# Kernel tuning notes

Hardware: AMD Instinct MI355X
Metric: run time of the kernel (lower is better)

Reference implementation:

```python
import jax, jax.numpy as jnp
import numpy as np

B, T, D, H = 256, 512, 512, 512


def setup_inputs() -> dict:
    key = jax.random.key(0)
    k1, k2, k3, k4 = jax.random.split(key, 4)
    inputs = jax.random.normal(k1, (B, T, D), dtype=jnp.float32)
    lengths = jax.random.randint(k2, (B,), 0, T).astype(jnp.int32)
    # LSTM params. Flax nn.LSTMCell uses per-gate dense layers:
    #  input dense (with bias) and recurrent dense (no bias). Packing the
    #  four gates (i, f, g, o) into one matrix is mathematically identical.
    Wx = jax.random.normal(k3, (D, 4 * H), dtype=jnp.float32) * (1.0 / np.sqrt(D))
    Wh = jax.random.normal(k4, (H, 4 * H), dtype=jnp.float32) * (1.0 / np.sqrt(H))
    b = jnp.zeros((4 * H,), dtype=jnp.float32)
    return {"inputs": inputs, "lengths": lengths, "Wx": Wx, "Wh": Wh, "b": b}


def reference(inputs, lengths, Wx, Wh, b):
    batch = inputs.shape[0]
    hidden = Wh.shape[0]
    x_tbd = jnp.swapaxes(inputs, 0, 1)  # [T, B, D]

    def step(carry, x_t):
        c, h = carry
        # fused gate pre-activations: [B, 4H]
        z = x_t @ Wx + h @ Wh + b
        i, f, g, o = jnp.split(z, 4, axis=-1)
        i = jax.nn.sigmoid(i)
        f = jax.nn.sigmoid(f)
        g = jnp.tanh(g)
        o = jax.nn.sigmoid(o)
        c_new = f * c + i * g
        h_new = o * jnp.tanh(c_new)
        return (c_new, h_new), h_new

    c0 = jnp.zeros((batch, hidden), dtype=inputs.dtype)
    h0 = jnp.zeros((batch, hidden), dtype=inputs.dtype)
    _, hs = jax.lax.scan(step, (c0, h0), x_tbd)  # hs: [T, B, H]

    # select output at last valid timestep per example
    idx = jnp.maximum(0, lengths - 1)  # [B]
    return hs[idx, jnp.arange(batch), :]  # [B, H]
```

## Files before the change

### kernel.cpp

```cpp
#include <hip/hip_runtime.h>

#define Bb 256
#define Tt 512
#define Dd 512
#define Hh 512
#define KTOT 1024
#define FOURH 2048

typedef __attribute__((ext_vector_type(8))) short bf16x8;
typedef __attribute__((ext_vector_type(4))) float f32x4;

__device__ __forceinline__ unsigned short f2bf(float f) {
    union { float f; unsigned u; } x; x.f = f;
    unsigned u = x.u;
    unsigned r = u + 0x7FFFu + ((u >> 16) & 1u);
    return (unsigned short)(r >> 16);
}
__device__ __forceinline__ float bf2f(unsigned short s) {
    union { unsigned u; float f; } x; x.u = ((unsigned)s) << 16;
    return x.f;
}

__device__ __forceinline__ uint4 load16_sc01(const void* p) {
    uint4 v;
    asm volatile("global_load_dwordx4 %0, %1, off sc0 sc1" : "=v"(v) : "v"(p));
    return v;
}

__device__ __forceinline__ void i16_to_bf(int v, unsigned short& bh, unsigned short& bl) {
    int vh = v >> 8;
    int vl = v & 255;
    union { float f; unsigned u; } a, b;
    a.f = (float)vh * 0.0078125f;
    b.f = (float)vl * 3.0517578125e-05f;
    bh = (unsigned short)(a.u >> 16);
    bl = (unsigned short)(b.u >> 16);
}

__global__ void prep_w(const float* __restrict__ Wx, const float* __restrict__ Wh,
                       unsigned short* __restrict__ WT_hi, unsigned short* __restrict__ WT_lo) {
    __shared__ float tile[32][33];
    int n0 = (blockIdx.x & 63) * 32;
    int k0 = (blockIdx.x >> 6) * 32;
    int tx = threadIdx.x & 31;
    int ty = threadIdx.x >> 5;
    for (int q = 0; q < 4; ++q) {
        int k = k0 + ty + q * 8;
        int n = n0 + tx;
        float v = (k < Dd) ? Wx[(size_t)k * FOURH + n] : Wh[(size_t)(k - Dd) * FOURH + n];
        tile[ty + q * 8][tx] = v;
    }
    __syncthreads();
    for (int q = 0; q < 4; ++q) {
        int nl = ty + q * 8;
        int kl = tx;
        float v = tile[kl][nl];
        unsigned short hi = f2bf(v);
        unsigned short lo = f2bf(v - bf2f(hi));
        size_t o = (size_t)(n0 + nl) * KTOT + (size_t)(k0 + kl);
        WT_hi[o] = hi;
        WT_lo[o] = lo;
    }
}

__global__ void init_state3(char* __restrict__ ws, int persist) {
    long i = (long)blockIdx.x * blockDim.x + threadIdx.x;
    if (i < 98304) {
        *(uint4*)(ws + (8u << 20) + i * 16) = (uint4){0, 0, 0, 0};
    }
    if (persist && i < 4096) {
        ((unsigned int*)(ws + (8u << 20) + (1536u << 10)))[i] = 0u;
    }
}

__global__ __launch_bounds__(512) void lstm_persist12(
    const float* __restrict__ X, const int* __restrict__ lengths,
    const unsigned short* __restrict__ WT_hi, const unsigned short* __restrict__ WT_lo,
    const float* __restrict__ bias,
    short* __restrict__ h_i16,
    unsigned int* __restrict__ ctrl,
    float* __restrict__ out)
{
    __shared__ unsigned short HLDS[32768];
    __shared__ unsigned short XLDS[32768];
    __shared__ float zbuf[8][32][17];

    const int bx = blockIdx.x;
    const int group = bx & 7;
    const int slot = bx >> 3;
    const int rt = slot & 7;
    const int cs = slot >> 3;
    const int r0 = rt * 32;
    const int j0h = group * 64 + cs * 16;
    const int tid = threadIdx.x;
    const int w8 = tid >> 6;
    const int lane = tid & 63;
    const int l15 = lane & 15;
    const int q4 = lane >> 4;
    const int klo = q4 * 8;
    const int gate = w8 & 3;
    const int khalf = w8 >> 2;

    const size_t HB = (size_t)Bb * Hh;

    const int colg = gate * 512 + j0h + l15;
    const size_t bbase = (size_t)colg * KTOT + (size_t)khalf * 512;
    const unsigned short* bhp = &WT_hi[bbase];
    const unsigned short* blp = &WT_lo[bbase];

    const int xr = tid >> 4;
    const int xk0 = (tid & 15) * 32;
    const float* xbase = &X[((size_t)(r0 + xr) * Tt) * Dd + xk0];
    const int ksx = tid & 15;
    const int xmi = xr >> 4, xlr = xr & 15;

    const int er = tid >> 4;
    const int ej = tid & 15;
    const int row_g = r0 + er;
    const int col_h = j0h + ej;
    const size_t oidx = (size_t)row_g * Hh + col_h;
    int oT = lengths[row_g] - 1; if (oT < 0) oT = 0;
    const float b0 = bias[col_h], b1 = bias[512 + col_h],
                b2 = bias[1024 + col_h], b3 = bias[1536 + col_h];
    float creg = 0.f;

    const int wgIdx = group * 4 + cs;
    unsigned int* myflag = ctrl + ((size_t)(rt * 32 + wgIdx)) * 16;
    const unsigned int* flagbase = ctrl + (size_t)rt * 32 * 16;
    const unsigned int* pollp = flagbase + (size_t)(lane & 31) * 16;

    {
        const float* xp = xbase;
        float4 xv[8];
#pragma unroll
        for (int i = 0; i < 8; ++i) xv[i] = ((const float4*)xp)[i];
#pragma unroll
        for (int c2 = 0; c2 < 4; ++c2) {
            float vv[8];
            *(float4*)&vv[0] = xv[2 * c2];
            *(float4*)&vv[4] = xv[2 * c2 + 1];
            bf16x8 hv8, lv8;
#pragma unroll
            for (int e = 0; e < 8; ++e) {
                unsigned short hs = f2bf(vv[e]);
                hv8[e] = (short)hs;
                lv8[e] = (short)f2bf(vv[e] - bf2f(hs));
            }
            const int lnw = (c2 * 16 + xlr) ^ (ksx & 7);
            *(bf16x8*)&XLDS[(((0 * 2 + xmi) * 16 + ksx) * 64 + lnw) * 8] = hv8;
            *(bf16x8*)&XLDS[(((1 * 2 + xmi) * 16 + ksx) * 64 + lnw) * 8] = lv8;
        }
    }

    for (int t = 0; t < Tt; ++t) {
        const int p_r = t & 1;
        const short* hp_r = h_i16 + (size_t)p_r * HB;
        short* hp_w = h_i16 + (size_t)(p_r ^ 1) * HB;

        uint4 hb[4];
#pragma unroll
        for (int it = 0; it < 4; ++it) {
            const int c = it * 512 + tid;
            const int row = c >> 6, k8 = c & 63;
            hb[it] = load16_sc01(hp_r + (size_t)(r0 + row) * Hh + k8 * 8);
        }

        asm volatile("s_waitcnt vmcnt(0)" ::: "memory");
        __builtin_amdgcn_sched_barrier(0);

#pragma unroll
        for (int it = 0; it < 4; ++it) {
            const int c = it * 512 + tid;
            const int row = c >> 6, k8 = c & 63;
            const int ksh = k8 >> 2, qq = k8 & 3;
            const int mi = row >> 4, lr = row & 15;
            const uint4 q = hb[it];
            const unsigned qs[4] = {q.x, q.y, q.z, q.w};
            bf16x8 ahv, alv;
#pragma unroll
            for (int e = 0; e < 4; ++e) {
                const unsigned u = qs[e];
                unsigned short bh0, bl0, bh1, bl1;
                i16_to_bf((int)(short)(u & 0xffffu), bh0, bl0);
                i16_to_bf((int)(short)(u >> 16), bh1, bl1);
                ahv[2 * e] = (short)bh0; alv[2 * e] = (short)bl0;
                ahv[2 * e + 1] = (short)bh1; alv[2 * e + 1] = (short)bl1;
            }
            const int lnw = (qq * 16 + lr) ^ (ksh & 7);
            *(bf16x8*)&HLDS[(((0 * 2 + mi) * 16 + ksh) * 64 + lnw) * 8] = ahv;
            *(bf16x8*)&HLDS[(((1 * 2 + mi) * 16 + ksh) * 64 + lnw) * 8] = alv;
        }
        __syncthreads();

        const unsigned short* ALDS = khalf ? HLDS : XLDS;
        f32x4 acc[2][3];
#pragma unroll
        for (int mi = 0; mi < 2; ++mi)
#pragma unroll
            for (int s = 0; s < 3; ++s)
                acc[mi][s] = (f32x4){0.f, 0.f, 0.f, 0.f};

#pragma unroll
        for (int ks = 0; ks < 16; ++ks) {
            const int kk = ks * 32 + klo;
            const bf16x8 bh = *(const bf16x8*)&bhp[kk];
            const bf16x8 bl = *(const bf16x8*)&blp[kk];
            const int lnr = lane ^ (ks & 7);
#pragma unroll
            for (int mi = 0; mi < 2; ++mi) {
                const bf16x8 ah = *(const bf16x8*)&ALDS[(((0 * 2 + mi) * 16 + ks) * 64 + lnr) * 8];
                const bf16x8 al = *(const bf16x8*)&ALDS[(((1 * 2 + mi) * 16 + ks) * 64 + lnr) * 8];
                acc[mi][0] = __builtin_amdgcn_mfma_f32_16x16x32_bf16(ah, bh, acc[mi][0], 0, 0, 0);
                acc[mi][1] = __builtin_amdgcn_mfma_f32_16x16x32_bf16(ah, bl, acc[mi][1], 0, 0, 0);
                acc[mi][2] = __builtin_amdgcn_mfma_f32_16x16x32_bf16(al, bh, acc[mi][2], 0, 0, 0);
            }
        }

#pragma unroll
        for (int mi = 0; mi < 2; ++mi) {
            const f32x4 z = acc[mi][0] + acc[mi][1] + acc[mi][2];
#pragma unroll
            for (int r = 0; r < 4; ++r)
                zbuf[w8][mi * 16 + q4 * 4 + r][l15] = z[r];
        }
        __syncthreads();

        float zi = zbuf[0][er][ej] + zbuf[4][er][ej] + b0;
        float zf = zbuf[1][er][ej] + zbuf[5][er][ej] + b1;
        float zg = zbuf[2][er][ej] + zbuf[6][er][ej] + b2;
        float zo = zbuf[3][er][ej] + zbuf[7][er][ej] + b3;
        float ig = 1.f / (1.f + expf(-zi));
        float fg = 1.f / (1.f + expf(-zf));
        float gg = tanhf(zg);
        float og = 1.f / (1.f + expf(-zo));
        float cn = fg * creg + ig * gg;
        creg = cn;
        float hn = og * tanhf(cn);
        int vi = __float2int_rn(hn * 32768.f);
        vi = vi > 32767 ? 32767 : (vi < -32767 ? -32767 : vi);
        __hip_atomic_store(&hp_w[oidx], (short)vi, __ATOMIC_RELAXED, __HIP_MEMORY_SCOPE_SYSTEM);
        if (t == oT) out[oidx] = hn;

        if (t < Tt - 1) {
            asm volatile("s_waitcnt vmcnt(0)" ::: "memory");
            __syncthreads();
            if (tid == 0)
                __hip_atomic_store(myflag, (unsigned)(t + 1), __ATOMIC_RELAXED,
                                   __HIP_MEMORY_SCOPE_SYSTEM);

            {
                const float* xp = xbase + (size_t)(t + 1) * Dd;
                float4 xv[8];
#pragma unroll
                for (int i = 0; i < 8; ++i) xv[i] = ((const float4*)xp)[i];
#pragma unroll
                for (int c2 = 0; c2 < 4; ++c2) {
                    float vv[8];
                    *(float4*)&vv[0] = xv[2 * c2];
                    *(float4*)&vv[4] = xv[2 * c2 + 1];
                    bf16x8 hv8, lv8;
#pragma unroll
                    for (int e = 0; e < 8; ++e) {
                        unsigned short hs = f2bf(vv[e]);
                        hv8[e] = (short)hs;
                        lv8[e] = (short)f2bf(vv[e] - bf2f(hs));
                    }
                    const int lnw = (c2 * 16 + xlr) ^ (ksx & 7);
                    *(bf16x8*)&XLDS[(((0 * 2 + xmi) * 16 + ksx) * 64 + lnw) * 8] = hv8;
                    *(bf16x8*)&XLDS[(((1 * 2 + xmi) * 16 + ksx) * 64 + lnw) * 8] = lv8;
                }
            }

            if (w8 == 0) {
                while (true) {
                    unsigned v = __hip_atomic_load(pollp, __ATOMIC_RELAXED,
                                                   __HIP_MEMORY_SCOPE_SYSTEM);
                    if (__all(v >= (unsigned)(t + 1))) break;
                    __builtin_amdgcn_s_sleep(2);
                }
            }
            __syncthreads();
        }
    }
}

__global__ __launch_bounds__(512) void lstm_step4(
    const float* __restrict__ X, const int* __restrict__ lengths,
    const unsigned short* __restrict__ WT_hi, const unsigned short* __restrict__ WT_lo,
    const float* __restrict__ bias,
    float* __restrict__ c_st,
    const unsigned short* __restrict__ h_r_hi, const unsigned short* __restrict__ h_r_lo,
    unsigned short* __restrict__ h_w_hi, unsigned short* __restrict__ h_w_lo,
    float* __restrict__ out, int t)
{
    __shared__ float zbuf[8][16][17];

    const int bx = blockIdx.x;
    const int xcd = bx & 7;
    const int rem = bx >> 3;
    const int m0 = (rem & 15) * 16;
    const int col_group = xcd * 4 + (rem >> 4);
    const int hc0 = col_group * 16;
    const int tid = threadIdx.x;
    const int w8 = tid >> 6;
    const int lane = tid & 63;
    const int gate = w8 & 3;
    const int khalf = w8 >> 2;

    f32x4 ahh = (f32x4){0,0,0,0}, ahl = (f32x4){0,0,0,0}, alh = (f32x4){0,0,0,0};

    const int colk = gate * 512 + hc0 + (lane & 15);
    const size_t bbase = (size_t)colk * KTOT;
    const int klo = (lane >> 4) * 8;
    const int row = m0 + (lane & 15);

    if (khalf == 0) {
        const float* xrow = &X[((size_t)row * Tt + t) * Dd];
        const unsigned short* bhp = &WT_hi[bbase];
        const unsigned short* blp = &WT_lo[bbase];
#pragma unroll
        for (int ks = 0; ks < 16; ++ks) {
            const int kk = ks * 32 + klo;
            const float4 v0 = *(const float4*)&xrow[kk];
            const float4 v1 = *(const float4*)&xrow[kk + 4];
            float vv[8] = {v0.x, v0.y, v0.z, v0.w, v1.x, v1.y, v1.z, v1.w};
            bf16x8 ah, al;
#pragma unroll
            for (int e = 0; e < 8; ++e) {
                unsigned short hi = f2bf(vv[e]);
                ah[e] = (short)hi;
                al[e] = (short)f2bf(vv[e] - bf2f(hi));
            }
            const bf16x8 bh = *(const bf16x8*)&bhp[kk];
            const bf16x8 bl = *(const bf16x8*)&blp[kk];
            ahh = __builtin_amdgcn_mfma_f32_16x16x32_bf16(ah, bh, ahh, 0, 0, 0);
            ahl = __builtin_amdgcn_mfma_f32_16x16x32_bf16(ah, bl, ahl, 0, 0, 0);
            alh = __builtin_amdgcn_mfma_f32_16x16x32_bf16(al, bh, alh, 0, 0, 0);
        }
    } else {
        const unsigned short* hrh = &h_r_hi[(size_t)row * Hh];
        const unsigned short* hrl = &h_r_lo[(size_t)row * Hh];
        const unsigned short* bhp = &WT_hi[bbase + 512];
        const unsigned short* blp = &WT_lo[bbase + 512];
#pragma unroll
        for (int ks = 0; ks < 16; ++ks) {
            const int kk = ks * 32 + klo;
            const bf16x8 ah = *(const bf16x8*)&hrh[kk];
            const bf16x8 al = *(const bf16x8*)&hrl[kk];
            const bf16x8 bh = *(const bf16x8*)&bhp[kk];
            const bf16x8 bl = *(const bf16x8*)&blp[kk];
            ahh = __builtin_amdgcn_mfma_f32_16x16x32_bf16(ah, bh, ahh, 0, 0, 0);
            ahl = __builtin_amdgcn_mfma_f32_16x16x32_bf16(ah, bl, ahl, 0, 0, 0);
            alh = __builtin_amdgcn_mfma_f32_16x16x32_bf16(al, bh, alh, 0, 0, 0);
        }
    }

    const f32x4 z = ahh + ahl + alh;
#pragma unroll
    for (int r = 0; r < 4; ++r)
        zbuf[w8][(lane >> 4) * 4 + r][lane & 15] = z[r];
    __syncthreads();

    if (tid < 256) {
        const int r = tid >> 4;
        const int j = tid & 15;
        const int row_g = m0 + r;
        const int col_g = hc0 + j;
        float zi = zbuf[0][r][j] + zbuf[4][r][j] + bias[col_g];
        float zf = zbuf[1][r][j] + zbuf[5][r][j] + bias[512 + col_g];
        float zg = zbuf[2][r][j] + zbuf[6][r][j] + bias[1024 + col_g];
        float zo = zbuf[3][r][j] + zbuf[7][r][j] + bias[1536 + col_g];
        float ig = 1.f / (1.f + expf(-zi));
        float fg = 1.f / (1.f + expf(-zf));
        float gg = tanhf(zg);
        float og = 1.f / (1.f + expf(-zo));
        const size_t idx = (size_t)row_g * Hh + col_g;
        float cn = fg * c_st[idx] + ig * gg;
        float hn = og * tanhf(cn);
        c_st[idx] = cn;
        unsigned short hh = f2bf(hn);
        h_w_hi[idx] = hh;
        h_w_lo[idx] = f2bf(hn - bf2f(hh));
        int len = lengths[row_g];
        int oidx = len - 1; if (oidx < 0) oidx = 0;
        if (t == oidx) out[idx] = hn;
    }
}

extern "C" void kernel_launch(void* const* d_in, const int* in_sizes, int n_in,
                              void* d_out, int out_size, void* d_ws, size_t ws_size,
                              hipStream_t stream) {
    const float* X = (const float*)d_in[0];
    const int* lengths = (const int*)d_in[1];
    const float* Wx = (const float*)d_in[2];
    const float* Wh = (const float*)d_in[3];
    const float* bias = (const float*)d_in[4];
    float* out = (float*)d_out;

    char* ws = (char*)d_ws;
    unsigned short* WT_hi = (unsigned short*)ws;
    unsigned short* WT_lo = (unsigned short*)(ws + (4u << 20));
    short* h_i16 = (short*)(ws + (8u << 20));
    unsigned int* ctrl = (unsigned int*)(ws + (8u << 20) + (1536u << 10));
    float* c_st = (float*)(ws + (8u << 20));
    unsigned short* h_base = (unsigned short*)(ws + (8u << 20) + (512u << 10));
    const size_t HB = (size_t)Bb * Hh;
    unsigned short* h_hi0 = h_base;
    unsigned short* h_lo0 = h_base + HB;
    unsigned short* h_hi1 = h_base + 2 * HB;
    unsigned short* h_lo1 = h_base + 3 * HB;

    const size_t NEED_PERSIST = (8u << 20) + (1536u << 10) + 32768u;
    const int can_persist = (ws_size >= NEED_PERSIST) ? 1 : 0;

    hipLaunchKernelGGL(prep_w, dim3(2048), dim3(256), 0, stream, Wx, Wh, WT_hi, WT_lo);
    hipLaunchKernelGGL(init_state3, dim3(512), dim3(256), 0, stream, ws, can_persist);

    hipError_t err = hipErrorUnknown;
    if (can_persist) {
        void* args[] = { (void*)&X, (void*)&lengths, (void*)&WT_hi, (void*)&WT_lo,
                         (void*)&bias, (void*)&h_i16, (void*)&ctrl, (void*)&out };
        err = hipLaunchCooperativeKernel((const void*)lstm_persist12,
                                         dim3(256), dim3(512), args, 0, stream);
    }
    if (err != hipSuccess) {
        for (int t = 0; t < Tt; ++t) {
            const bool even = (t & 1) == 0;
            hipLaunchKernelGGL(lstm_step4, dim3(512), dim3(512), 0, stream,
                               X, lengths, WT_hi, WT_lo, bias, c_st,
                               even ? h_hi0 : h_hi1, even ? h_lo0 : h_lo1,
                               even ? h_hi1 : h_hi0, even ? h_lo1 : h_lo0,
                               out, t);
        }
    }
}
```

Baseline: 6.112 ms.

## Halve batch rows per workgroup and launch twice as many persistent blocks

The persistent LSTM kernel now gives each workgroup 16 batch rows instead of 32 and launches 512 cooperative blocks instead of 256, shrinking the LDS buffers and MFMA accumulators to match. Each step's per-block work (h load, X conversion, one MFMA tile per wave) is halved, so more CUs share the serial recurrence. In exchange there are twice as many flags to poll and sync across blocks, half the threads sit idle during the gate math, and each block reloads the same weight slice for less work. The launch bound of 4 blocks per CU is set so the cooperative grid can be co-resident.

Result: slower. 8.250 ms (+35.0%).

```diff
diff --git a/kernel.cpp b/kernel.cpp
--- a/kernel.cpp
+++ b/kernel.cpp
@@ -68,12 +68,12 @@
     if (i < 98304) {
         *(uint4*)(ws + (8u << 20) + i * 16) = (uint4){0, 0, 0, 0};
     }
-    if (persist && i < 4096) {
+    if (persist && i < 8192) {
         ((unsigned int*)(ws + (8u << 20) + (1536u << 10)))[i] = 0u;
     }
 }
 
-__global__ __launch_bounds__(512) void lstm_persist12(
+__global__ __launch_bounds__(512, 4) void lstm_persist18(
     const float* __restrict__ X, const int* __restrict__ lengths,
     const unsigned short* __restrict__ WT_hi, const unsigned short* __restrict__ WT_lo,
     const float* __restrict__ bias,
@@ -81,16 +81,15 @@
     unsigned int* __restrict__ ctrl,
     float* __restrict__ out)
 {
-    __shared__ unsigned short HLDS[32768];
-    __shared__ unsigned short XLDS[32768];
-    __shared__ float zbuf[8][32][17];
+    __shared__ unsigned short HLDS[16384];
+    __shared__ unsigned short XLDS[16384];
+    __shared__ float zbuf[8][16][17];
 
     const int bx = blockIdx.x;
     const int group = bx & 7;
-    const int slot = bx >> 3;
-    const int rt = slot & 7;
-    const int cs = slot >> 3;
-    const int r0 = rt * 32;
+    const int cs = (bx >> 3) & 3;
+    const int rt = bx >> 5;
+    const int r0 = rt * 16;
     const int j0h = group * 64 + cs * 16;
     const int tid = threadIdx.x;
     const int w8 = tid >> 6;
@@ -108,18 +107,17 @@
     const unsigned short* bhp = &WT_hi[bbase];
     const unsigned short* blp = &WT_lo[bbase];
 
-    const int xr = tid >> 4;
-    const int xk0 = (tid & 15) * 32;
-    const float* xbase = &X[((size_t)(r0 + xr) * Tt) * Dd + xk0];
-    const int ksx = tid & 15;
-    const int xmi = xr >> 4, xlr = xr & 15;
-
-    const int er = tid >> 4;
+    const int xr = tid >> 5;
+    const int xs = tid & 31;
+    const float* xbase = &X[((size_t)(r0 + xr) * Tt) * Dd + xs * 16];
+
+    const int er = (tid >> 4) & 15;
     const int ej = tid & 15;
     const int row_g = r0 + er;
     const int col_h = j0h + ej;
     const size_t oidx = (size_t)row_g * Hh + col_h;
-    int oT = lengths[row_g] - 1; if (oT < 0) oT = 0;
+    int oT = 0;
+    if (tid < 256) { oT = lengths[row_g] - 1; if (oT < 0) oT = 0; }
     const float b0 = bias[col_h], b1 = bias[512 + col_h],
                 b2 = bias[1024 + col_h], b3 = bias[1536 + col_h];
     float creg = 0.f;
@@ -131,11 +129,11 @@
 
     {
         const float* xp = xbase;
-        float4 xv[8];
-#pragma unroll
-        for (int i = 0; i < 8; ++i) xv[i] = ((const float4*)xp)[i];
-#pragma unroll
-        for (int c2 = 0; c2 < 4; ++c2) {
+        float4 xv[4];
+#pragma unroll
+        for (int i = 0; i < 4; ++i) xv[i] = ((const float4*)xp)[i];
+#pragma unroll
+        for (int c2 = 0; c2 < 2; ++c2) {
             float vv[8];
             *(float4*)&vv[0] = xv[2 * c2];
             *(float4*)&vv[4] = xv[2 * c2 + 1];
@@ -146,9 +144,12 @@
                 hv8[e] = (short)hs;
                 lv8[e] = (short)f2bf(vv[e] - bf2f(hs));
             }
-            const int lnw = (c2 * 16 + xlr) ^ (ksx & 7);
-            *(bf16x8*)&XLDS[(((0 * 2 + xmi) * 16 + ksx) * 64 + lnw) * 8] = hv8;
-            *(bf16x8*)&XLDS[(((1 * 2 + xmi) * 16 + ksx) * 64 + lnw) * 8] = lv8;
+            const int k = xs * 16 + c2 * 8;
+            const int ks = k >> 5;
+            const int qq = (k >> 3) & 3;
+            const int lnw = (qq * 16 + xr) ^ (ks & 7);
+            *(bf16x8*)&XLDS[((0 * 16 + ks) * 64 + lnw) * 8] = hv8;
+            *(bf16x8*)&XLDS[((1 * 16 + ks) * 64 + lnw) * 8] = lv8;
         }
     }
 
@@ -157,9 +158,9 @@
         const short* hp_r = h_i16 + (size_t)p_r * HB;
         short* hp_w = h_i16 + (size_t)(p_r ^ 1) * HB;
 
-        uint4 hb[4];
-#pragma unroll
-        for (int it = 0; it < 4; ++it) {
+        uint4 hb[2];
+#pragma unroll
+        for (int it = 0; it < 2; ++it) {
             const int c = it * 512 + tid;
             const int row = c >> 6, k8 = c & 63;
             hb[it] = load16_sc01(hp_r + (size_t)(r0 + row) * Hh + k8 * 8);
@@ -169,11 +170,10 @@
         __builtin_amdgcn_sched_barrier(0);
 
 #pragma unroll
-        for (int it = 0; it < 4; ++it) {
+        for (int it = 0; it < 2; ++it) {
             const int c = it * 512 + tid;
             const int row = c >> 6, k8 = c & 63;
             const int ksh = k8 >> 2, qq = k8 & 3;
-            const int mi = row >> 4, lr = row & 15;
             const uint4 q = hb[it];
             const unsigned qs[4] = {q.x, q.y, q.z, q.w};
             bf16x8 ahv, alv;
@@ -186,60 +186,53 @@
                 ahv[2 * e] = (short)bh0; alv[2 * e] = (short)bl0;
                 ahv[2 * e + 1] = (short)bh1; alv[2 * e + 1] = (short)bl1;
             }
-            const int lnw = (qq * 16 + lr) ^ (ksh & 7);
-            *(bf16x8*)&HLDS[(((0 * 2 + mi) * 16 + ksh) * 64 + lnw) * 8] = ahv;
-            *(bf16x8*)&HLDS[(((1 * 2 + mi) * 16 + ksh) * 64 + lnw) * 8] = alv;
+            const int lnw = (qq * 16 + row) ^ (ksh & 7);
+            *(bf16x8*)&HLDS[((0 * 16 + ksh) * 64 + lnw) * 8] = ahv;
+            *(bf16x8*)&HLDS[((1 * 16 + ksh) * 64 + lnw) * 8] = alv;
         }
         __syncthreads();
 
-        const unsigned short* ALDS = khalf ? HLDS : XLDS;
-        f32x4 acc[2][3];
-#pragma unroll
-        for (int mi = 0; mi < 2; ++mi)
-#pragma unroll
-            for (int s = 0; s < 3; ++s)
-                acc[mi][s] = (f32x4){0.f, 0.f, 0.f, 0.f};
-
+        const unsigned short* ALDSs = khalf ? HLDS : XLDS;
+        f32x4 acc0 = (f32x4){0, 0, 0, 0};
+        f32x4 acc1 = (f32x4){0, 0, 0, 0};
+        f32x4 acc2 = (f32x4){0, 0, 0, 0};
 #pragma unroll
         for (int ks = 0; ks < 16; ++ks) {
             const int kk = ks * 32 + klo;
             const bf16x8 bh = *(const bf16x8*)&bhp[kk];
             const bf16x8 bl = *(const bf16x8*)&blp[kk];
             const int lnr = lane ^ (ks & 7);
-#pragma unroll
-            for (int mi = 0; mi < 2; ++mi) {
-                const bf16x8 ah = *(const bf16x8*)&ALDS[(((0 * 2 + mi) * 16 + ks) * 64 + lnr) * 8];
-                const bf16x8 al = *(const bf16x8*)&ALDS[(((1 * 2 + mi) * 16 + ks) * 64 + lnr) * 8];
-                acc[mi][0] = __builtin_amdgcn_mfma_f32_16x16x32_bf16(ah, bh, acc[mi][0], 0, 0, 0);
-                acc[mi][1] = __builtin_amdgcn_mfma_f32_16x16x32_bf16(ah, bl, acc[mi][1], 0, 0, 0);
-                acc[mi][2] = __builtin_amdgcn_mfma_f32_16x16x32_bf16(al, bh, acc[mi][2], 0, 0, 0);
-            }
-        }
-
-#pragma unroll
-        for (int mi = 0; mi < 2; ++mi) {
-            const f32x4 z = acc[mi][0] + acc[mi][1] + acc[mi][2];
+            const bf16x8 ah = *(const bf16x8*)&ALDSs[((0 * 16 + ks) * 64 + lnr) * 8];
+            const bf16x8 al = *(const bf16x8*)&ALDSs[((1 * 16 + ks) * 64 + lnr) * 8];
+            acc0 = __builtin_amdgcn_mfma_f32_16x16x32_bf16(ah, bh, acc0, 0, 0, 0);
+            acc1 = __builtin_amdgcn_mfma_f32_16x16x32_bf16(ah, bl, acc1, 0, 0, 0);
+            acc2 = __builtin_amdgcn_mfma_f32_16x16x32_bf16(al, bh, acc2, 0, 0, 0);
+        }
+        {
+            const f32x4 z = acc0 + acc1 + acc2;
 #pragma unroll
             for (int r = 0; r < 4; ++r)
-                zbuf[w8][mi * 16 + q4 * 4 + r][l15] = z[r];
+                zbuf[w8][q4 * 4 + r][l15] = z[r];
         }
         __syncthreads();
 
-        float zi = zbuf[0][er][ej] + zbuf[4][er][ej] + b0;
-        float zf = zbuf[1][er][ej] + zbuf[5][er][ej] + b1;
-        float zg = zbuf[2][er][ej] + zbuf[6][er][ej] + b2;
-        float zo = zbuf[3][er][ej] + zbuf[7][er][ej] + b3;
-        float ig = 1.f / (1.f + expf(-zi));
-        float fg = 1.f / (1.f + expf(-zf));
-        float gg = tanhf(zg);
-        float og = 1.f / (1.f + expf(-zo));
-        float cn = fg * creg + ig * gg;
-        creg = cn;
-        float hn = og * tanhf(cn);
-        int vi = __float2int_rn(hn * 32768.f);
-        vi = vi > 32767 ? 32767 : (vi < -32767 ? -32767 : vi);
-        __hip_atomic_store(&hp_w[oidx], (short)vi, __ATOMIC_RELAXED, __HIP_MEMORY_SCOPE_SYSTEM);
-        if (t == oT) out[oidx] = hn;
+        if (tid < 256) {
+            float zi = zbuf[0][er][ej] + zbuf[4][er][ej] + b0;
+            float zf = zbuf[1][er][ej] + zbuf[5][er][ej] + b1;
+            float zg = zbuf[2][er][ej] + zbuf[6][er][ej] + b2;
+            float zo = zbuf[3][er][ej] + zbuf[7][er][ej] + b3;
+            float ig = 1.f / (1.f + expf(-zi));
+            float fg = 1.f / (1.f + expf(-zf));
+            float gg = tanhf(zg);
+            float og = 1.f / (1.f + expf(-zo));
+            float cn = fg * creg + ig * gg;
+            creg = cn;
+            float hn = og * tanhf(cn);
+            int vi = __float2int_rn(hn * 32768.f);
+            vi = vi > 32767 ? 32767 : (vi < -32767 ? -32767 : vi);
+            __hip_atomic_store(&hp_w[oidx], (short)vi, __ATOMIC_RELAXED, __HIP_MEMORY_SCOPE_SYSTEM);
+            if (t == oT) out[oidx] = hn;
+        }
 
         if (t < Tt - 1) {
             asm volatile("s_waitcnt vmcnt(0)" ::: "memory");
@@ -250,11 +243,11 @@
 
             {
                 const float* xp = xbase + (size_t)(t + 1) * Dd;
-                float4 xv[8];
-#pragma unroll
-                for (int i = 0; i < 8; ++i) xv[i] = ((const float4*)xp)[i];
-#pragma unroll
-                for (int c2 = 0; c2 < 4; ++c2) {
+                float4 xv[4];
+#pragma unroll
+                for (int i = 0; i < 4; ++i) xv[i] = ((const float4*)xp)[i];
+#pragma unroll
+                for (int c2 = 0; c2 < 2; ++c2) {
                     float vv[8];
                     *(float4*)&vv[0] = xv[2 * c2];
                     *(float4*)&vv[4] = xv[2 * c2 + 1];
@@ -265,9 +258,12 @@
                         hv8[e] = (short)hs;
                         lv8[e] = (short)f2bf(vv[e] - bf2f(hs));
                     }
-                    const int lnw = (c2 * 16 + xlr) ^ (ksx & 7);
-                    *(bf16x8*)&XLDS[(((0 * 2 + xmi) * 16 + ksx) * 64 + lnw) * 8] = hv8;
-                    *(bf16x8*)&XLDS[(((1 * 2 + xmi) * 16 + ksx) * 64 + lnw) * 8] = lv8;
+                    const int k = xs * 16 + c2 * 8;
+                    const int ks = k >> 5;
+                    const int qq = (k >> 3) & 3;
+                    const int lnw = (qq * 16 + xr) ^ (ks & 7);
+                    *(bf16x8*)&XLDS[((0 * 16 + ks) * 64 + lnw) * 8] = hv8;
+                    *(bf16x8*)&XLDS[((1 * 16 + ks) * 64 + lnw) * 8] = lv8;
                 }
             }
 
@@ -410,7 +406,7 @@
     unsigned short* h_hi1 = h_base + 2 * HB;
     unsigned short* h_lo1 = h_base + 3 * HB;
 
-    const size_t NEED_PERSIST = (8u << 20) + (1536u << 10) + 32768u;
+    const size_t NEED_PERSIST = (8u << 20) + (1536u << 10) + 65536u;
     const int can_persist = (ws_size >= NEED_PERSIST) ? 1 : 0;
 
     hipLaunchKernelGGL(prep_w, dim3(2048), dim3(256), 0, stream, Wx, Wh, WT_hi, WT_lo);
@@ -420,8 +416,8 @@
     if (can_persist) {
         void* args[] = { (void*)&X, (void*)&lengths, (void*)&WT_hi, (void*)&WT_lo,
                          (void*)&bias, (void*)&h_i16, (void*)&ctrl, (void*)&out };
-        err = hipLaunchCooperativeKernel((const void*)lstm_persist12,
-                                         dim3(256), dim3(512), args, 0, stream);
+        err = hipLaunchCooperativeKernel((const void*)lstm_persist18,
+                                         dim3(512), dim3(512), args, 0, stream);
     }
     if (err != hipSuccess) {
         for (int t = 0; t < Tt; ++t) {
```
